# Kernel tuning notes

Hardware: AMD Instinct MI355X
Metric: run time of the kernel (lower is better)

## Reference

```python
import jax, jax.numpy as jnp
import numpy as np

LAMDA = 0.5  # weight between agent-selected hidden state and current hidden state
SAMPLE_SEED = 42  # RNG for categorical action sampling (torch version is stochastic)


def setup_inputs() -> dict:
    B, T, D, H, U, A = 256, 512, 128, 128, 64, 10
    key = jax.random.key(0)
    ks = jax.random.split(key, 16)
    s = 0.1
    return {
        "x": jax.random.normal(ks[0], (B, T, D), dtype=jnp.float32),
        "mask": jnp.ones((B, T), dtype=jnp.int32),
        # GRUCell params (torch layout: [3H, in], gate order r,z,n)
        "gru_w_ih": jax.random.normal(ks[1], (3 * H, D), dtype=jnp.float32) * s,
        "gru_w_hh": jax.random.normal(ks[2], (3 * H, H), dtype=jnp.float32) * s,
        "gru_b_ih": jnp.zeros((3 * H,), dtype=jnp.float32),
        "gru_b_hh": jnp.zeros((3 * H,), dtype=jnp.float32),
        # agent1 MLP: observes mean of hidden buffer ([B,H])
        "a1_w1": jax.random.normal(ks[3], (U, H), dtype=jnp.float32) * s,
        "a1_b1": jnp.zeros((U,), dtype=jnp.float32),
        "a1_w2": jax.random.normal(ks[4], (A, U), dtype=jnp.float32) * s,
        "a1_b2": jnp.zeros((A,), dtype=jnp.float32),
        # agent2 MLP: observes current input ([B,D])
        "a2_w1": jax.random.normal(ks[5], (U, D), dtype=jnp.float32) * s,
        "a2_b1": jnp.zeros((U,), dtype=jnp.float32),
        "a2_w2": jax.random.normal(ks[6], (A, U), dtype=jnp.float32) * s,
        "a2_b2": jnp.zeros((A,), dtype=jnp.float32),
    }


def _gru_cell(xt, h, w_ih, w_hh, b_ih, b_hh):
    gi = xt @ w_ih.T + b_ih  # [B, 3H]
    gh = h @ w_hh.T + b_hh
    ir, iz, inn = jnp.split(gi, 3, axis=-1)
    hr, hz, hn = jnp.split(gh, 3, axis=-1)
    r = jax.nn.sigmoid(ir + hr)
    z = jax.nn.sigmoid(iz + hz)
    n = jnp.tanh(inn + r * hn)
    return (1.0 - z) * n + z * h


def _agent_action(obs, w1, b1, w2, b2, key):
    # observation is detached in the original (choose_action detaches)
    z = jnp.tanh(jax.lax.stop_gradient(obs) @ w1.T + b1)
    logits = z @ w2.T + b2  # Categorical(softmax(logits)) == categorical over logits
    return jax.random.categorical(key, logits, axis=-1)  # [B]


def reference(x, mask, gru_w_ih, gru_w_hh, gru_b_ih, gru_b_hh,
              a1_w1, a1_b1, a1_w2, a1_b2, a2_w1, a2_b1, a2_w2, a2_b2):
    B, T, D = x.shape
    H = gru_w_hh.shape[1]
    A = a1_w2.shape[0]
    keys = jax.random.split(jax.random.key(SAMPLE_SEED), 2 * T).reshape(T, 2)

    gru = lambda xt, h: _gru_cell(xt, h, gru_w_ih, gru_w_hh, gru_b_ih, gru_b_hh)

    # t == 0: cur_h is zeros, action_h == cur_h, so weighted_h == 0; agent samples
    # at t=0 are discarded for state (they only fill RL bookkeeping lists).
    h0 = gru(x[:, 0], jnp.zeros((B, H), x.dtype))
    buf0 = jnp.zeros((A, B, H), x.dtype)  # observed_h history buffer
    bidx = jnp.arange(B)

    def step(carry, inp):
        h, buf = carry
        xt, kt = inp
        buf = jnp.concatenate([buf[1:], h[None]], axis=0)  # shift in previous hidden
        a1 = _agent_action(buf.mean(axis=0), a1_w1, a1_b1, a1_w2, a1_b2, kt[0])
        a2 = _agent_action(xt, a2_w1, a2_b1, a2_w2, a2_b2, kt[1])
        action_h = (buf[a1, bidx] + buf[a2, bidx]) * 0.5  # [B,H] gather of past states
        weighted_h = LAMDA * action_h + (1.0 - LAMDA) * h
        hn = gru(xt, weighted_h)
        return (hn, buf), hn

    xs = (jnp.swapaxes(x[:, 1:], 0, 1), keys[1:])  # time-major
    _, hs = jax.lax.scan(step, (h0, buf0), xs)
    h_all = jnp.swapaxes(jnp.concatenate([h0[None], hs], axis=0), 0, 1)  # [B,T,H]

    last_idx = jnp.sum(mask, axis=1) - 1  # get_last_visit
    last_out = h_all[bidx, last_idx]  # [B,H]; dropout=0.0 -> identity
    return last_out, h_all
```

## Files before the change

kernel.cpp:

```cpp
#include <hip/hip_runtime.h>
#include <math.h>

#define B_ 256
#define T_ 512
#define D_ 128
#define H_ 128
#define BH_ 32768
#define NG 1308160

__device__ __forceinline__ void bar_lds() {
  asm volatile("s_waitcnt lgkmcnt(0)\n\ts_barrier" ::: "memory");
}

__device__ __forceinline__ float dpp_add_xor1(float v) {
  int r = __builtin_amdgcn_update_dpp(0, __float_as_int(v), 0xB1, 0xF, 0xF, true);
  return v + __int_as_float(r);
}
__device__ __forceinline__ float dpp_add_xor2(float v) {
  int r = __builtin_amdgcn_update_dpp(0, __float_as_int(v), 0x4E, 0xF, 0xF, true);
  return v + __int_as_float(r);
}

__device__ __forceinline__ float frcp(float x) { return __builtin_amdgcn_rcpf(x); }
__device__ __forceinline__ float fsigmoid(float x) { return frcp(1.0f + __expf(-x)); }
__device__ __forceinline__ float ftanh_(float x) { return 1.0f - 2.0f * frcp(1.0f + __expf(2.0f * x)); }

__device__ __forceinline__ void tf2x32(unsigned k0, unsigned k1, unsigned x0, unsigned x1,
                                       unsigned& o0, unsigned& o1) {
  unsigned k2 = k0 ^ k1 ^ 0x1BD11BDAu;
  unsigned v0 = x0 + k0, v1 = x1 + k1;
#define TFR(r) { v0 += v1; v1 = (v1 << (r)) | (v1 >> (32 - (r))); v1 ^= v0; }
  TFR(13) TFR(15) TFR(26) TFR(6)   v0 += k1; v1 += k2 + 1u;
  TFR(17) TFR(29) TFR(16) TFR(24)  v0 += k2; v1 += k0 + 2u;
  TFR(13) TFR(15) TFR(26) TFR(6)   v0 += k0; v1 += k1 + 3u;
  TFR(17) TFR(29) TFR(16) TFR(24)  v0 += k1; v1 += k2 + 4u;
  TFR(13) TFR(15) TFR(26) TFR(6)   v0 += k2; v1 += k0 + 5u;
#undef TFR
  o0 = v0; o1 = v1;
}

__device__ __forceinline__ float gumbel_f(unsigned bits) {
  const float tiny = 1.17549435e-38f;
  float u = __uint_as_float((bits >> 9) | 0x3f800000u) - 1.0f;
  u = u + tiny;
  u = fmaxf(tiny, u);
  return -__logf(-__logf(u));
}

__global__ void p0_keys(unsigned* __restrict__ keys_tab) {
  int i = blockIdx.x * blockDim.x + threadIdx.x;
  if (i >= 1024) return;
  unsigned o0, o1;
  tf2x32(0u, 42u, 0u, (unsigned)i, o0, o1);
  keys_tab[2 * i] = o0; keys_tab[2 * i + 1] = o1;
}

#define SX 264
#define SW 72
__global__ __launch_bounds__(256, 4) void gemm_tiled(
    const float* __restrict__ x, const float* __restrict__ w_ih,
    const float* __restrict__ b_ih, const float* __restrict__ a2w1,
    const float* __restrict__ a2b1, float* __restrict__ gi, float* __restrict__ zt) {
  __shared__ __align__(16) float Xs[32 * SX];
  __shared__ __align__(16) float Ws[32 * SW];
  const int tid = threadIdx.x;
  const int mb = blockIdx.x & 511;
  const int nb = blockIdx.x >> 9;
  const bool isz = (nb == 6);
  const size_t m0 = (size_t)mb * 256;
  const int n0 = isz ? 0 : nb * 64;
  const float* wsrc = isz ? a2w1 : w_ih;
  const float* bsrc = isz ? a2b1 : b_ih;
  const int mt = tid >> 4;
  const int nt = tid & 15;
  const int kg = tid >> 5;
  const int ri = tid & 31;

  float acc[16][4];
  #pragma unroll
  for (int i = 0; i < 16; i++)
    #pragma unroll
    for (int j = 0; j < 4; j++) acc[i][j] = 0.f;

  #pragma unroll 1
  for (int kc = 0; kc < 4; kc++) {
    const int k0 = kc * 32;
    __syncthreads();
    #pragma unroll
    for (int p = 0; p < 8; p++) {
      int row = ri + 32 * p;
      float4 v = *(const float4*)(x + (m0 + row) * 128 + k0 + 4 * kg);
      Xs[(4 * kg + 0) * SX + row] = v.x;
      Xs[(4 * kg + 1) * SX + row] = v.y;
      Xs[(4 * kg + 2) * SX + row] = v.z;
      Xs[(4 * kg + 3) * SX + row] = v.w;
    }
    #pragma unroll
    for (int p = 0; p < 2; p++) {
      int n = ri + 32 * p;
      float4 v = *(const float4*)(wsrc + (size_t)(n0 + n) * 128 + k0 + 4 * kg);
      Ws[(4 * kg + 0) * SW + n] = v.x;
      Ws[(4 * kg + 1) * SW + n] = v.y;
      Ws[(4 * kg + 2) * SW + n] = v.z;
      Ws[(4 * kg + 3) * SW + n] = v.w;
    }
    __syncthreads();
    #pragma unroll 4
    for (int kk = 0; kk < 32; kk++) {
      const float* xrow = Xs + kk * SX + mt * 16;
      float4 xa0 = ((const float4*)xrow)[0];
      float4 xa1 = ((const float4*)xrow)[1];
      float4 xa2 = ((const float4*)xrow)[2];
      float4 xa3 = ((const float4*)xrow)[3];
      float4 wv = *(const float4*)(Ws + kk * SW + nt * 4);
      float xv[16] = {xa0.x, xa0.y, xa0.z, xa0.w, xa1.x, xa1.y, xa1.z, xa1.w,
                      xa2.x, xa2.y, xa2.z, xa2.w, xa3.x, xa3.y, xa3.z, xa3.w};
      #pragma unroll
      for (int i = 0; i < 16; i++) {
        acc[i][0] += xv[i] * wv.x;
        acc[i][1] += xv[i] * wv.y;
        acc[i][2] += xv[i] * wv.z;
        acc[i][3] += xv[i] * wv.w;
      }
    }
  }
  float4 bias = *(const float4*)(bsrc + n0 + nt * 4);
  if (!isz) {
    #pragma unroll
    for (int i = 0; i < 16; i++) {
      float4 o;
      o.x = acc[i][0] + bias.x; o.y = acc[i][1] + bias.y;
      o.z = acc[i][2] + bias.z; o.w = acc[i][3] + bias.w;
      size_t m = m0 + (size_t)mt * 16 + i;
      *(float4*)(gi + m * 384 + n0 + nt * 4) = o;
    }
  } else {
    #pragma unroll
    for (int i = 0; i < 16; i++) {
      float4 o;
      o.x = ftanh_(acc[i][0] + bias.x); o.y = ftanh_(acc[i][1] + bias.y);
      o.z = ftanh_(acc[i][2] + bias.z); o.w = ftanh_(acc[i][3] + bias.w);
      size_t m = m0 + (size_t)mt * 16 + i;
      *(float4*)(zt + m * 64 + nt * 4) = o;
    }
  }
}

__global__ __launch_bounds__(256) void sampler(
    const float* __restrict__ zt, const float* __restrict__ w2,
    const float* __restrict__ b2, const unsigned* __restrict__ keys_tab,
    float* __restrict__ g1, int* __restrict__ a2_tab) {
  __shared__ __align__(16) float w2s[10][64];
  __shared__ float b2s[10];
  __shared__ __align__(16) float zs[4][64];
  const int tid = threadIdx.x, w = tid >> 6, lane = tid & 63;
  const int t = blockIdx.x + 1;
  for (int i = tid; i < 640; i += 256) w2s[i >> 6][i & 63] = w2[i];
  if (tid < 10) b2s[tid] = b2[tid];
  __syncthreads();
  const unsigned k0a = keys_tab[2 * (2 * t + 1)], k1a = keys_tab[2 * (2 * t + 1) + 1];
  const unsigned k0g = keys_tab[2 * (2 * t)],     k1g = keys_tab[2 * (2 * t) + 1];
  const int a = lane & 15, kc = lane >> 4;
  float zr = zt[((size_t)w * 512 + t) * 64 + lane];
  #pragma unroll 1
  for (int it = 0; it < 64; it++) {
    const int b = 4 * it + w;
    zs[w][lane] = zr;
    if (it < 63) zr = zt[((size_t)(b + 4) * 512 + t) * 64 + lane];
    float p = 0.f;
    if (a < 10) {
      const float4* zp = (const float4*)(&zs[w][16 * kc]);
      const float4* wp = (const float4*)(&w2s[a][16 * kc]);
      #pragma unroll
      for (int c = 0; c < 4; c++) {
        float4 zv = zp[c], w4 = wp[c];
        p += w4.x * zv.x + w4.y * zv.y + w4.z * zv.z + w4.w * zv.w;
      }
    }
    p += __shfl_xor(p, 16);
    p += __shfl_xor(p, 32);
    float val = -3.0e38f;
    if (a < 10 && kc == 0) {
      unsigned o0, o1;
      tf2x32(k0a, k1a, 0u, (unsigned)(b * 10 + a), o0, o1);
      val = (p + b2s[a]) + gumbel_f(o0 ^ o1);
      tf2x32(k0g, k1g, 0u, (unsigned)(b * 10 + a), o0, o1);
      g1[((size_t)(t - 1) * 256 + b) * 10 + a] = gumbel_f(o0 ^ o1);
    }
    float best = 0.f; int bi = 0;
    #pragma unroll
    for (int aa = 0; aa < 10; aa++) {
      float v = __shfl(val, aa);
      if (aa == 0 || v > best) { best = v; bi = aa; }
    }
    if (lane == 0) a2_tab[(size_t)(t - 1) * 256 + b] = bi;
  }
}

__global__ __launch_bounds__(512, 2) void seq_kernel(
    const float* __restrict__ gi_glob, const int* __restrict__ mask,
    const float* __restrict__ w_hh, const float* __restrict__ b_hh,
    const float* __restrict__ a1w1, const float* __restrict__ a1b1,
    const float* __restrict__ a1w2, const float* __restrict__ a1b2,
    const float* __restrict__ g1_tab, const int* __restrict__ a2_tab,
    float* __restrict__ out) {
  __shared__ __align__(16) float ring2[20][128];
  __shared__ __align__(16) float yc[10][384];
  __shared__ __align__(16) float hbuf[128];
  __shared__ __align__(16) float ghi[384];
  __shared__ __align__(16) float obs[128];
  __shared__ __align__(16) float z1buf[64];
  __shared__ __align__(16) float lastbuf[128];
  __shared__ __align__(16) float w2buf[10][64];
  __shared__ float bhh3s[128];
  __shared__ float b1s[64], b2s[10];
  __shared__ float g1buf[10];
  __shared__ float2 pl2[16];
  __shared__ int a2s_lds;
  __shared__ int redi[8];
  __shared__ int last_s;

  const int tid = threadIdx.x;
  const int wave = tid >> 6, lane = tid & 63;
  const int b = blockIdx.x;

  float4 wr[4][8];
  const int q = tid >> 2, qk = tid & 3;
  if (tid < 384) {
    #pragma unroll
    for (int i = 0; i < 4; i++) {
      const float* basep = w_hh + (size_t)(4 * q + i) * 128 + 4 * qk;
      #pragma unroll
      for (int c = 0; c < 8; c++) wr[i][c] = *(const float4*)(basep + 16 * c);
    }
  }
  float4 w1reg[16];
  float4 bhh4a = make_float4(0.f, 0.f, 0.f, 0.f);
  if (wave >= 6) {
    int m = ((wave - 6) << 5) + (lane >> 1);
    int kc = lane & 1;
    const float4* wp = (const float4*)(a1w1 + (size_t)m * 128 + 64 * kc);
    #pragma unroll
    for (int c = 0; c < 16; c++) w1reg[c] = wp[c];
  }
  if (wave == 6) bhh4a = ((const float4*)b_hh)[lane];

  for (int idx = tid; idx < 2560; idx += 512) ((float*)ring2)[idx] = 0.f;
  for (int idx = tid; idx < 3840; idx += 512) ((float*)yc)[idx] = 0.f;
  for (int idx = tid; idx < 640; idx += 512) w2buf[idx >> 6][idx & 63] = a1w2[idx];
  if (tid < 128) bhh3s[tid] = b_hh[256 + tid];
  if (tid < 64) b1s[tid] = a1b1[tid];
  if (tid < 10) b2s[tid] = a1b2[tid];
  int mv = mask[(size_t)b * T_ + tid];
  #pragma unroll
  for (int off = 1; off < 64; off <<= 1) mv += __shfl_xor(mv, off);
  if (lane == 0) redi[wave] = mv;
  const float4* gi4 = (const float4*)gi_glob;
  float4 gir0 = make_float4(0.f, 0.f, 0.f, 0.f), gir1 = gir0;
  if (wave == 6) {
    size_t base1 = ((size_t)b * 512 + 1) * 96;
    gir0 = gi4[base1 + lane];
    if (lane < 32) gir1 = gi4[base1 + 64 + lane];
  }
  float g1r = 0.f; int a2r = 0;
  if (wave == 7 && lane < 10) g1r = g1_tab[(size_t)b * 10 + lane];
  if (wave == 7 && lane == 12) a2r = a2_tab[b];
  __syncthreads();
  if (tid == 0) {
    int s = 0;
    #pragma unroll
    for (int w = 0; w < 8; w++) s += redi[w];
    last_s = s - 1;
  }
  __syncthreads();
  const int last = last_s;

  if (tid < 128) {
    int j = tid;
    const float* g0 = gi_glob + (size_t)b * 512 * 384;
    float r  = fsigmoid(g0[j] + b_hh[j]);
    float zz = fsigmoid(g0[128 + j] + b_hh[128 + j]);
    float n  = ftanh_(g0[256 + j] + r * b_hh[256 + j]);
    float hnew = (1.0f - zz) * n;
    hbuf[j] = hnew; ring2[0][j] = hnew; ring2[10][j] = hnew;
    obs[j] = hnew / 10.0f;
    out[BH_ + ((size_t)b * 512) * 128 + j] = hnew;
    if (0 == last) lastbuf[j] = hnew;
  }
  __syncthreads();

  #pragma unroll 1
  for (int t = 1; t < T_; t++) {
    const int sn = (t + 9) % 10;
    if (tid < 384) {
      const float4* hb4 = (const float4*)hbuf;
      float4 a0 = make_float4(0.f, 0.f, 0.f, 0.f), a1v = a0, a2v = a0, a3v = a0;
      #pragma unroll
      for (int c = 0; c < 8; c++) {
        float4 h4 = hb4[4 * c + qk];
        a0.x += wr[0][c].x * h4.x; a0.y += wr[0][c].y * h4.y; a0.z += wr[0][c].z * h4.z; a0.w += wr[0][c].w * h4.w;
        a1v.x += wr[1][c].x * h4.x; a1v.y += wr[1][c].y * h4.y; a1v.z += wr[1][c].z * h4.z; a1v.w += wr[1][c].w * h4.w;
        a2v.x += wr[2][c].x * h4.x; a2v.y += wr[2][c].y * h4.y; a2v.z += wr[2][c].z * h4.z; a2v.w += wr[2][c].w * h4.w;
        a3v.x += wr[3][c].x * h4.x; a3v.y += wr[3][c].y * h4.y; a3v.z += wr[3][c].z * h4.z; a3v.w += wr[3][c].w * h4.w;
      }
      float s0  = (a0.x + a0.y) + (a0.z + a0.w);
      float s1v = (a1v.x + a1v.y) + (a1v.z + a1v.w);
      float s2v = (a2v.x + a2v.y) + (a2v.z + a2v.w);
      float s3v = (a3v.x + a3v.y) + (a3v.z + a3v.w);
      s0  = dpp_add_xor2(dpp_add_xor1(s0));
      s1v = dpp_add_xor2(dpp_add_xor1(s1v));
      s2v = dpp_add_xor2(dpp_add_xor1(s2v));
      s3v = dpp_add_xor2(dpp_add_xor1(s3v));
      float my = (qk == 0) ? s0 : (qk == 1) ? s1v : (qk == 2) ? s2v : s3v;
      yc[sn][4 * q + qk] = my;
    } else if (wave == 6) {
      float4 g0 = gir0;
      g0.x += bhh4a.x; g0.y += bhh4a.y; g0.z += bhh4a.z; g0.w += bhh4a.w;
      ((float4*)ghi)[lane] = g0;
      if (lane < 32) ((float4*)ghi)[64 + lane] = gir1;
      if (t < 511) {
        size_t basep = ((size_t)b * 512 + t + 1) * 96;
        gir0 = gi4[basep + lane];
        if (lane < 32) gir1 = gi4[basep + 64 + lane];
      }
      {
        int m = lane >> 1, kc = lane & 1;
        float ax = 0.f, ay = 0.f, az = 0.f, aw = 0.f;
        #pragma unroll
        for (int c = 0; c < 16; c++) {
          float4 o4 = ((const float4*)obs)[16 * kc + c];
          ax += w1reg[c].x * o4.x; ay += w1reg[c].y * o4.y;
          az += w1reg[c].z * o4.z; aw += w1reg[c].w * o4.w;
        }
        float d = (ax + ay) + (az + aw);
        d = dpp_add_xor1(d);
        if (kc == 0) z1buf[m] = ftanh_(d + b1s[m]);
      }
      if (lane < 40) {
        int a = lane >> 2, k2 = lane & 3;
        int m0 = 8 * k2;
        float4 z4a = ((const float4*)(z1buf + m0))[0], z4b = ((const float4*)(z1buf + m0))[1];
        float4 wa = ((const float4*)(&w2buf[a][m0]))[0], wb = ((const float4*)(&w2buf[a][m0]))[1];
        float p = z4a.x * wa.x + z4a.y * wa.y + z4a.z * wa.z + z4a.w * wa.w
                + z4b.x * wb.x + z4b.y * wb.y + z4b.z * wb.z + z4b.w * wb.w;
        p = dpp_add_xor2(dpp_add_xor1(p));
        if (k2 == 0) pl2[a].x = p + b2s[a];
      }
    } else {
      if (lane < 10) g1buf[lane] = g1r;
      if (lane == 12) a2s_lds = a2r;
      if (t < 511) {
        if (lane < 10) g1r = g1_tab[((size_t)t * 256 + b) * 10 + lane];
        if (lane == 12) a2r = a2_tab[(size_t)t * 256 + b];
      }
      {
        int m = 32 + (lane >> 1), kc = lane & 1;
        float ax = 0.f, ay = 0.f, az = 0.f, aw = 0.f;
        #pragma unroll
        for (int c = 0; c < 16; c++) {
          float4 o4 = ((const float4*)obs)[16 * kc + c];
          ax += w1reg[c].x * o4.x; ay += w1reg[c].y * o4.y;
          az += w1reg[c].z * o4.z; aw += w1reg[c].w * o4.w;
        }
        float d = (ax + ay) + (az + aw);
        d = dpp_add_xor1(d);
        if (kc == 0) z1buf[m] = ftanh_(d + b1s[m]);
      }
      if (lane < 40) {
        int a = lane >> 2, k2 = lane & 3;
        int m0 = 32 + 8 * k2;
        float4 z4a = ((const float4*)(z1buf + m0))[0], z4b = ((const float4*)(z1buf + m0))[1];
        float4 wa = ((const float4*)(&w2buf[a][m0]))[0], wb = ((const float4*)(&w2buf[a][m0]))[1];
        float p = z4a.x * wa.x + z4a.y * wa.y + z4a.z * wa.z + z4a.w * wa.w
                + z4b.x * wb.x + z4b.y * wb.y + z4b.z * wb.z + z4b.w * wb.w;
        p = dpp_add_xor2(dpp_add_xor1(p));
        if (k2 == 0) pl2[a].y = p + g1buf[a];
      }
    }
    bar_lds();

    if (tid < 128) {
      float best = 0.f; int bi = 0;
      #pragma unroll
      for (int a = 0; a < 10; a++) {
        float2 pv = pl2[a];
        float v = pv.x + pv.y;
        if (a == 0 || v > best) { best = v; bi = a; }
      }
      const int s1 = (t + bi) % 10;
      const int s2 = (t + a2s_lds) % 10;
      int j = tid;
      float gh1 = 0.5f * (0.5f * (yc[s1][j]       + yc[s2][j]))       + 0.5f * yc[sn][j];
      float gh2 = 0.5f * (0.5f * (yc[s1][128 + j] + yc[s2][128 + j])) + 0.5f * yc[sn][128 + j];
      float gh3 = bhh3s[j] + 0.5f * (0.5f * (yc[s1][256 + j] + yc[s2][256 + j])) + 0.5f * yc[sn][256 + j];
      float r  = fsigmoid(ghi[j] + gh1);
      float zz = fsigmoid(ghi[128 + j] + gh2);
      float n  = ftanh_(ghi[256 + j] + r * gh3);
      float hw = 0.5f * ((ring2[s1][j] + ring2[s2][j]) * 0.5f) + 0.5f * hbuf[j];
      float hnew = (1.0f - zz) * n + zz * hw;
      hbuf[j] = hnew;
      ring2[t % 10][j] = hnew;
      ring2[t % 10 + 10][j] = hnew;
      out[BH_ + ((size_t)b * 512 + t) * 128 + j] = hnew;
      if (t == last) lastbuf[j] = hnew;
      int base = (t + 1) % 10;
      float s = 0.f;
      #pragma unroll
      for (int a = 0; a < 9; a++) s += ring2[base + a][j];
      s += hnew;
      obs[j] = s / 10.0f;
    }
    bar_lds();
  }
  if (tid < 128) out[(size_t)b * H_ + tid] = lastbuf[tid];
}

extern "C" void kernel_launch(void* const* d_in, const int* in_sizes, int n_in,
                              void* d_out, int out_size, void* d_ws, size_t ws_size,
                              hipStream_t stream) {
  (void)in_sizes; (void)n_in; (void)out_size; (void)ws_size;
  const float* x     = (const float*)d_in[0];
  const int*   mask  = (const int*)d_in[1];
  const float* w_ih  = (const float*)d_in[2];
  const float* w_hh  = (const float*)d_in[3];
  const float* b_ih  = (const float*)d_in[4];
  const float* b_hh  = (const float*)d_in[5];
  const float* a1w1  = (const float*)d_in[6];
  const float* a1b1  = (const float*)d_in[7];
  const float* a1w2  = (const float*)d_in[8];
  const float* a1b2  = (const float*)d_in[9];
  const float* a2w1  = (const float*)d_in[10];
  const float* a2b1  = (const float*)d_in[11];
  const float* a2w2  = (const float*)d_in[12];
  const float* a2b2  = (const float*)d_in[13];
  float* out = (float*)d_out;

  float*    gi       = (float*)d_ws;
  float*    g1       = gi + (size_t)131072 * 384;
  unsigned* keys_tab = (unsigned*)(g1 + NG);
  int*      a2_tab   = (int*)(keys_tab + 2048);
  float*    zt       = (float*)(a2_tab + 130816);

  p0_keys<<<4, 256, 0, stream>>>(keys_tab);
  gemm_tiled<<<3584, 256, 0, stream>>>(x, w_ih, b_ih, a2w1, a2b1, gi, zt);
  sampler<<<511, 256, 0, stream>>>(zt, a2w2, a2b2, keys_tab, g1, a2_tab);
  seq_kernel<<<256, 512, 0, stream>>>(gi, mask, w_hh, b_hh,
                                      a1w1, a1b1, a1w2, a1b2, g1, a2_tab, out);
}
```

Measured before the change: 1.088 ms.

## Interleave gate layout, spread tail phase across waves, offload obs sum, double-buffer prefetch

The hidden-projection results and input gates are stored interleaved per hidden unit, so the tail phase reads each with a single float4 load. The tail work is spread over 32 lanes in each of 4 waves instead of 2 full waves. The 9-term ring sum for the observation mean is moved to waves 6 and 7, which would otherwise sit idle before the barrier. Prefetch of gi, g1 and a2 now runs two steps ahead using alternating register sets, and the step loop is unrolled by two. Modulo arithmetic is replaced by a running counter, and the last-visit output is written directly instead of going through an LDS buffer. The changes shorten the serial critical path of each timestep, at the cost of more registers and a more complex schedule.

```diff
diff --git a/kernel.cpp b/kernel.cpp
--- a/kernel.cpp
+++ b/kernel.cpp
@@ -150,7 +150,7 @@
     const float* __restrict__ zt, const float* __restrict__ w2,
     const float* __restrict__ b2, const unsigned* __restrict__ keys_tab,
     float* __restrict__ g1, int* __restrict__ a2_tab) {
-  __shared__ __align__(16) float w2s[10][64];
+  __shared__ __align__(16) float w2s[10][68];
   __shared__ float b2s[10];
   __shared__ __align__(16) float zs[4][64];
   const int tid = threadIdx.x, w = tid >> 6, lane = tid & 63;
@@ -205,27 +205,26 @@
     const float* __restrict__ g1_tab, const int* __restrict__ a2_tab,
     float* __restrict__ out) {
   __shared__ __align__(16) float ring2[20][128];
-  __shared__ __align__(16) float yc[10][384];
+  __shared__ __align__(16) float yct[10][512];
+  __shared__ __align__(16) float ghi4[512];
   __shared__ __align__(16) float hbuf[128];
-  __shared__ __align__(16) float ghi[384];
   __shared__ __align__(16) float obs[128];
+  __shared__ __align__(16) float osum[128];
   __shared__ __align__(16) float z1buf[64];
-  __shared__ __align__(16) float lastbuf[128];
-  __shared__ __align__(16) float w2buf[10][64];
-  __shared__ float bhh3s[128];
+  __shared__ __align__(16) float w2buf[10][68];
   __shared__ float b1s[64], b2s[10];
   __shared__ float g1buf[10];
-  __shared__ float2 pl2[16];
+  __shared__ __align__(16) float2 pl2[16];
   __shared__ int a2s_lds;
   __shared__ int redi[8];
   __shared__ int last_s;
 
   const int tid = threadIdx.x;
-  const int wave = tid >> 6, lane = tid & 63;
+  const int wv = tid >> 6, lane = tid & 63;
   const int b = blockIdx.x;
+  const int q = tid >> 2, qk = tid & 3;
 
   float4 wr[4][8];
-  const int q = tid >> 2, qk = tid & 3;
   if (tid < 384) {
     #pragma unroll
     for (int i = 0; i < 4; i++) {
@@ -235,36 +234,45 @@
     }
   }
   float4 w1reg[16];
-  float4 bhh4a = make_float4(0.f, 0.f, 0.f, 0.f);
-  if (wave >= 6) {
-    int m = ((wave - 6) << 5) + (lane >> 1);
+  if (wv >= 6) {
+    int m = ((wv - 6) << 5) + (lane >> 1);
     int kc = lane & 1;
     const float4* wp = (const float4*)(a1w1 + (size_t)m * 128 + 64 * kc);
     #pragma unroll
     for (int c = 0; c < 16; c++) w1reg[c] = wp[c];
   }
-  if (wave == 6) bhh4a = ((const float4*)b_hh)[lane];
+  float bhh6[6] = {0.f, 0.f, 0.f, 0.f, 0.f, 0.f};
+  float gA[6] = {0.f, 0.f, 0.f, 0.f, 0.f, 0.f};
+  float gB[6] = {0.f, 0.f, 0.f, 0.f, 0.f, 0.f};
+  float g1A = 0.f, g1B = 0.f;
+  int a2A = 0, a2B = 0;
+  if (wv == 6) {
+    bhh6[0] = b_hh[lane];       bhh6[1] = b_hh[128 + lane]; bhh6[2] = b_hh[256 + lane];
+    bhh6[3] = b_hh[64 + lane];  bhh6[4] = b_hh[192 + lane]; bhh6[5] = b_hh[320 + lane];
+    size_t p1 = ((size_t)b * 512 + 1) * 384;
+    gA[0] = gi_glob[p1 + lane];      gA[1] = gi_glob[p1 + 128 + lane]; gA[2] = gi_glob[p1 + 256 + lane];
+    gA[3] = gi_glob[p1 + 64 + lane]; gA[4] = gi_glob[p1 + 192 + lane]; gA[5] = gi_glob[p1 + 320 + lane];
+    size_t p2 = ((size_t)b * 512 + 2) * 384;
+    gB[0] = gi_glob[p2 + lane];      gB[1] = gi_glob[p2 + 128 + lane]; gB[2] = gi_glob[p2 + 256 + lane];
+    gB[3] = gi_glob[p2 + 64 + lane]; gB[4] = gi_glob[p2 + 192 + lane]; gB[5] = gi_glob[p2 + 320 + lane];
+  }
+  if (wv == 7) {
+    if (lane < 10) {
+      g1A = g1_tab[(size_t)b * 10 + lane];
+      g1B = g1_tab[((size_t)1 * 256 + b) * 10 + lane];
+    }
+    if (lane == 12) { a2A = a2_tab[b]; a2B = a2_tab[256 + b]; }
+  }
 
   for (int idx = tid; idx < 2560; idx += 512) ((float*)ring2)[idx] = 0.f;
-  for (int idx = tid; idx < 3840; idx += 512) ((float*)yc)[idx] = 0.f;
+  for (int idx = tid; idx < 5120; idx += 512) ((float*)yct)[idx] = 0.f;
   for (int idx = tid; idx < 640; idx += 512) w2buf[idx >> 6][idx & 63] = a1w2[idx];
-  if (tid < 128) bhh3s[tid] = b_hh[256 + tid];
   if (tid < 64) b1s[tid] = a1b1[tid];
   if (tid < 10) b2s[tid] = a1b2[tid];
   int mv = mask[(size_t)b * T_ + tid];
   #pragma unroll
   for (int off = 1; off < 64; off <<= 1) mv += __shfl_xor(mv, off);
-  if (lane == 0) redi[wave] = mv;
-  const float4* gi4 = (const float4*)gi_glob;
-  float4 gir0 = make_float4(0.f, 0.f, 0.f, 0.f), gir1 = gir0;
-  if (wave == 6) {
-    size_t base1 = ((size_t)b * 512 + 1) * 96;
-    gir0 = gi4[base1 + lane];
-    if (lane < 32) gir1 = gi4[base1 + 64 + lane];
-  }
-  float g1r = 0.f; int a2r = 0;
-  if (wave == 7 && lane < 10) g1r = g1_tab[(size_t)b * 10 + lane];
-  if (wave == 7 && lane == 12) a2r = a2_tab[b];
+  if (lane == 0) redi[wv] = mv;
   __syncthreads();
   if (tid == 0) {
     int s = 0;
@@ -275,8 +283,9 @@
   __syncthreads();
   const int last = last_s;
 
-  if (tid < 128) {
-    int j = tid;
+  float hprev = 0.f;
+  if (wv < 4 && lane < 32) {
+    const int j = (wv << 5) + lane;
     const float* g0 = gi_glob + (size_t)b * 512 * 384;
     float r  = fsigmoid(g0[j] + b_hh[j]);
     float zz = fsigmoid(g0[128 + j] + b_hh[128 + j]);
@@ -285,13 +294,15 @@
     hbuf[j] = hnew; ring2[0][j] = hnew; ring2[10][j] = hnew;
     obs[j] = hnew / 10.0f;
     out[BH_ + ((size_t)b * 512) * 128 + j] = hnew;
-    if (0 == last) lastbuf[j] = hnew;
-  }
-  __syncthreads();
-
-  #pragma unroll 1
-  for (int t = 1; t < T_; t++) {
-    const int sn = (t + 9) % 10;
+    if (0 == last) out[(size_t)b * H_ + j] = hnew;
+    hprev = hnew;
+  }
+  bar_lds();
+
+  int tmod = 1;
+
+  auto step = [&](int t, float (&gr)[6], float& g1r, int& a2r) {
+    const int sn = (tmod == 0) ? 9 : tmod - 1;
     if (tid < 384) {
       const float4* hb4 = (const float4*)hbuf;
       float4 a0 = make_float4(0.f, 0.f, 0.f, 0.f), a1v = a0, a2v = a0, a3v = a0;
@@ -312,16 +323,17 @@
       s2v = dpp_add_xor2(dpp_add_xor1(s2v));
       s3v = dpp_add_xor2(dpp_add_xor1(s3v));
       float my = (qk == 0) ? s0 : (qk == 1) ? s1v : (qk == 2) ? s2v : s3v;
-      yc[sn][4 * q + qk] = my;
-    } else if (wave == 6) {
-      float4 g0 = gir0;
-      g0.x += bhh4a.x; g0.y += bhh4a.y; g0.z += bhh4a.z; g0.w += bhh4a.w;
-      ((float4*)ghi)[lane] = g0;
-      if (lane < 32) ((float4*)ghi)[64 + lane] = gir1;
-      if (t < 511) {
-        size_t basep = ((size_t)b * 512 + t + 1) * 96;
-        gir0 = gi4[basep + lane];
-        if (lane < 32) gir1 = gi4[basep + 64 + lane];
+      yct[sn][((tid & 127) << 2) + (tid >> 7)] = my;
+    } else if (wv == 6) {
+      float4 e0, e1;
+      e0.x = gr[0] + bhh6[0]; e0.y = gr[1] + bhh6[1]; e0.z = gr[2]; e0.w = bhh6[2];
+      e1.x = gr[3] + bhh6[3]; e1.y = gr[4] + bhh6[4]; e1.z = gr[5]; e1.w = bhh6[5];
+      ((float4*)ghi4)[lane] = e0;
+      ((float4*)ghi4)[64 + lane] = e1;
+      if (t + 2 <= 511) {
+        size_t bp = ((size_t)b * 512 + t + 2) * 384;
+        gr[0] = gi_glob[bp + lane];      gr[1] = gi_glob[bp + 128 + lane]; gr[2] = gi_glob[bp + 256 + lane];
+        gr[3] = gi_glob[bp + 64 + lane]; gr[4] = gi_glob[bp + 192 + lane]; gr[5] = gi_glob[bp + 320 + lane];
       }
       {
         int m = lane >> 1, kc = lane & 1;
@@ -346,12 +358,19 @@
         p = dpp_add_xor2(dpp_add_xor1(p));
         if (k2 == 0) pl2[a].x = p + b2s[a];
       }
+      {
+        int bs = tmod + 1; if (bs >= 10) bs -= 10;
+        float s = 0.f;
+        #pragma unroll
+        for (int a = 0; a < 9; a++) s += ring2[bs + a][lane];
+        osum[lane] = s;
+      }
     } else {
       if (lane < 10) g1buf[lane] = g1r;
       if (lane == 12) a2s_lds = a2r;
-      if (t < 511) {
-        if (lane < 10) g1r = g1_tab[((size_t)t * 256 + b) * 10 + lane];
-        if (lane == 12) a2r = a2_tab[(size_t)t * 256 + b];
+      if (t + 2 <= 511) {
+        if (lane < 10) g1r = g1_tab[((size_t)(t + 1) * 256 + b) * 10 + lane];
+        if (lane == 12) a2r = a2_tab[(size_t)(t + 1) * 256 + b];
       }
       {
         int m = 32 + (lane >> 1), kc = lane & 1;
@@ -376,43 +395,61 @@
         p = dpp_add_xor2(dpp_add_xor1(p));
         if (k2 == 0) pl2[a].y = p + g1buf[a];
       }
+      {
+        int bs = tmod + 1; if (bs >= 10) bs -= 10;
+        float s = 0.f;
+        #pragma unroll
+        for (int a = 0; a < 9; a++) s += ring2[bs + a][64 + lane];
+        osum[64 + lane] = s;
+      }
     }
     bar_lds();
 
-    if (tid < 128) {
-      float best = 0.f; int bi = 0;
+    if (wv < 4 && lane < 32) {
+      const int j = (wv << 5) + lane;
+      float4 p0 = ((const float4*)pl2)[0];
+      float4 p1 = ((const float4*)pl2)[1];
+      float4 p2 = ((const float4*)pl2)[2];
+      float4 p3 = ((const float4*)pl2)[3];
+      float4 p4 = ((const float4*)pl2)[4];
+      int a2v = a2s_lds;
+      float l[10] = {p0.x + p0.y, p0.z + p0.w, p1.x + p1.y, p1.z + p1.w, p2.x + p2.y,
+                     p2.z + p2.w, p3.x + p3.y, p3.z + p3.w, p4.x + p4.y, p4.z + p4.w};
+      float best = l[0]; int bi = 0;
       #pragma unroll
-      for (int a = 0; a < 10; a++) {
-        float2 pv = pl2[a];
-        float v = pv.x + pv.y;
-        if (a == 0 || v > best) { best = v; bi = a; }
-      }
-      const int s1 = (t + bi) % 10;
-      const int s2 = (t + a2s_lds) % 10;
-      int j = tid;
-      float gh1 = 0.5f * (0.5f * (yc[s1][j]       + yc[s2][j]))       + 0.5f * yc[sn][j];
-      float gh2 = 0.5f * (0.5f * (yc[s1][128 + j] + yc[s2][128 + j])) + 0.5f * yc[sn][128 + j];
-      float gh3 = bhh3s[j] + 0.5f * (0.5f * (yc[s1][256 + j] + yc[s2][256 + j])) + 0.5f * yc[sn][256 + j];
-      float r  = fsigmoid(ghi[j] + gh1);
-      float zz = fsigmoid(ghi[128 + j] + gh2);
-      float n  = ftanh_(ghi[256 + j] + r * gh3);
-      float hw = 0.5f * ((ring2[s1][j] + ring2[s2][j]) * 0.5f) + 0.5f * hbuf[j];
+      for (int a = 1; a < 10; a++) { if (l[a] > best) { best = l[a]; bi = a; } }
+      int s1 = tmod + bi;  if (s1 >= 10) s1 -= 10;
+      int s2 = tmod + a2v; if (s2 >= 10) s2 -= 10;
+      float4 y1 = *(const float4*)(&yct[s1][j << 2]);
+      float4 y2 = *(const float4*)(&yct[s2][j << 2]);
+      float4 yn = *(const float4*)(&yct[sn][j << 2]);
+      float4 gv = ((const float4*)ghi4)[j];
+      float gh1 = 0.5f * (0.5f * (y1.x + y2.x)) + 0.5f * yn.x;
+      float gh2 = 0.5f * (0.5f * (y1.y + y2.y)) + 0.5f * yn.y;
+      float gh3 = gv.w + 0.5f * (0.5f * (y1.z + y2.z)) + 0.5f * yn.z;
+      float r  = fsigmoid(gv.x + gh1);
+      float zz = fsigmoid(gv.y + gh2);
+      float n  = ftanh_(gv.z + r * gh3);
+      float hw = 0.5f * ((ring2[s1][j] + ring2[s2][j]) * 0.5f) + 0.5f * hprev;
       float hnew = (1.0f - zz) * n + zz * hw;
       hbuf[j] = hnew;
-      ring2[t % 10][j] = hnew;
-      ring2[t % 10 + 10][j] = hnew;
+      ring2[tmod][j] = hnew;
+      ring2[tmod + 10][j] = hnew;
+      obs[j] = (osum[j] + hnew) / 10.0f;
       out[BH_ + ((size_t)b * 512 + t) * 128 + j] = hnew;
-      if (t == last) lastbuf[j] = hnew;
-      int base = (t + 1) % 10;
-      float s = 0.f;
-      #pragma unroll
-      for (int a = 0; a < 9; a++) s += ring2[base + a][j];
-      s += hnew;
-      obs[j] = s / 10.0f;
+      if (t == last) out[(size_t)b * H_ + j] = hnew;
+      hprev = hnew;
     }
     bar_lds();
-  }
-  if (tid < 128) out[(size_t)b * H_ + tid] = lastbuf[tid];
+    tmod = (tmod == 9) ? 0 : tmod + 1;
+  };
+
+  #pragma unroll 1
+  for (int t = 1; t < 511; t += 2) {
+    step(t, gA, g1A, a2A);
+    step(t + 1, gB, g1B, a2B);
+  }
+  step(511, gA, g1A, a2A);
 }
 
 extern "C" void kernel_launch(void* const* d_in, const int* in_sizes, int n_in,
```

New measurement: 1.570 ms. 44.3% more time.
